# Kernel optimization log

Measured on AMD Instinct MI355X. Metric: run time of the kernel, lower is better.

The kernel has to match this reference:

```python
import jax, jax.numpy as jnp
import numpy as np

N = 2_000_000
H = 50
N_MID = 7  # number of Linear(50,50)+Tanh blocks


def setup_inputs() -> dict:
    key = jax.random.key(0)
    ks = jax.random.split(key, 9)
    s = 0.1  # small init scale to keep tanh out of saturation
    return {
        "x": jax.random.normal(ks[0], (N, 1), jnp.float32),
        "y": jax.random.normal(ks[1], (N, 1), jnp.float32),
        "z": jax.random.normal(ks[2], (N, 1), jnp.float32),
        "W_in": jax.random.normal(ks[3], (3, H), jnp.float32) * s,
        "b_in": jax.random.normal(ks[4], (H,), jnp.float32) * s,
        "W_mid": jax.random.normal(ks[5], (N_MID, H, H), jnp.float32) * s,
        "b_mid": jax.random.normal(ks[6], (N_MID, H), jnp.float32) * s,
        "W_out": jax.random.normal(ks[7], (H, 3), jnp.float32) * s,
        "b_out": jax.random.normal(ks[8], (3,), jnp.float32) * s,
    }


def reference(x, y, z, W_in, b_in, W_mid, b_mid, W_out, b_out):
    # Uin = hstack(x, y, z) -> [N, 3]
    Uin = jnp.concatenate([x, y, z], axis=1)
    h = jnp.tanh(Uin @ W_in + b_in)            # [N, 50]
    for i in range(N_MID):                      # fixed small layer count
        h = jnp.tanh(h @ W_mid[i] + b_mid[i])   # [N, 50]
    U = h @ W_out + b_out                       # [N, 3]
    return (U[:, 0:1], U[:, 1:2], U[:, 2:3])
```

## Files before the change

kernel.cpp:

```cpp
#include <hip/hip_runtime.h>

#define HID 50
#define NMID 7
#define NT 4
#define NS 2
#define PT 4

#define MID_ELEMS (NMID * NT * NS * 64 * 8)
#define IN_ELEMS  (NT * 64 * 8)
#define OUT_ELEMS (NS * 64 * 8)
#define W_HALFS   (MID_ELEMS + IN_ELEMS + OUT_ELEMS)

#define SCALE 2.8853900817779268f

typedef _Float16 half8  __attribute__((ext_vector_type(8)));
typedef float    f32x4  __attribute__((ext_vector_type(4)));

__device__ __forceinline__ unsigned short f16hi(float w) {
    _Float16 h = (_Float16)w;
    return __builtin_bit_cast(unsigned short, h);
}
__device__ __forceinline__ unsigned short f16lo(float w) {
    _Float16 h = (_Float16)w;
    _Float16 l = (_Float16)(w - (float)h);
    return __builtin_bit_cast(unsigned short, l);
}

__device__ __forceinline__ int kperm(int k) {
    int s = k >> 5, q = (k >> 3) & 3, j = k & 7;
    return 16 * (2 * s + (j >> 2)) + 4 * q + (j & 3);
}

__global__ void pack_params(const float* __restrict__ W_in, const float* __restrict__ b_in,
                            const float* __restrict__ W_mid, const float* __restrict__ b_mid,
                            const float* __restrict__ W_out, const float* __restrict__ b_out,
                            unsigned short* __restrict__ wp) {
    int e = blockIdx.x * 256 + threadIdx.x;
    if (e < MID_ELEMS) {
        int L = e / (NT * NS * 512), r1 = e % (NT * NS * 512);
        int t = r1 / (NS * 512),     r2 = r1 % (NS * 512);
        int s = r2 / 512,            r3 = r2 % 512;
        int l = r3 / 8,              j  = r3 % 8;
        int fo = t * 16 + (l & 15);
        int k  = s * 32 + ((l >> 4) << 3) + j;
        unsigned short bits = 0;
        if (fo < HID) {
            if (k == 62)      bits = f16hi(SCALE * b_mid[L * HID + fo]);
            else if (k == 63) bits = f16lo(SCALE * b_mid[L * HID + fo]);
            else {
                int fi = kperm(k);
                if (fi < HID) bits = f16hi(SCALE * W_mid[(L * HID + fi) * HID + fo]);
            }
        }
        wp[e] = bits;
    } else if (e < MID_ELEMS + IN_ELEMS) {
        int e2 = e - MID_ELEMS;
        int t = e2 / 512, r = e2 % 512, l = r / 8, j = r % 8;
        int fo = t * 16 + (l & 15);
        int q  = l >> 4;
        unsigned short bits = 0;
        if (fo < HID && q == 0) {
            if (j < 3)       bits = f16hi(SCALE * W_in[j * HID + fo]);
            else if (j < 6)  bits = f16hi(SCALE * W_in[(j - 3) * HID + fo]);
            else if (j == 6) bits = f16hi(SCALE * b_in[fo]);
            else             bits = f16lo(SCALE * b_in[fo]);
        }
        wp[e] = bits;
    } else if (e < W_HALFS) {
        int e3 = e - MID_ELEMS - IN_ELEMS;
        int s = e3 / 512, r = e3 % 512, l = r / 8, j = r % 8;
        int m = l & 15;
        int k = s * 32 + ((l >> 4) << 3) + j;
        unsigned short bits = 0;
        if (m < 3) {
            if (k == 62)      bits = f16hi(b_out[m]);
            else if (k == 63) bits = f16lo(b_out[m]);
            else {
                int fi = kperm(k);
                if (fi < HID) bits = f16hi(W_out[fi * 3 + m]);
            }
        }
        wp[e] = bits;
    }
}

__device__ __forceinline__ float tanh_e(float a) {
    float e = __builtin_amdgcn_exp2f(a);
    float r = __builtin_amdgcn_rcpf(e + 1.0f);
    return __builtin_fmaf(r, -2.0f, 1.0f);
}
__device__ __forceinline__ unsigned int pk2(float a, float b) {
    auto p = __builtin_amdgcn_cvt_pkrtz(a, b);
    return __builtin_bit_cast(unsigned int, p);
}
__device__ __forceinline__ half8 epi_full(const f32x4& c0, const f32x4& c1) {
    uint4 u;
    u.x = pk2(tanh_e(c0[0]), tanh_e(c0[1]));
    u.y = pk2(tanh_e(c0[2]), tanh_e(c0[3]));
    u.z = pk2(tanh_e(c1[0]), tanh_e(c1[1]));
    u.w = pk2(tanh_e(c1[2]), tanh_e(c1[3]));
    return __builtin_bit_cast(half8, u);
}
__device__ __forceinline__ half8 epi_tail(const f32x4& c2, const f32x4& c3) {
    uint4 u;
    u.x = pk2(tanh_e(c2[0]), tanh_e(c2[1]));
    u.y = pk2(tanh_e(c2[2]), tanh_e(c2[3]));
    u.z = pk2(tanh_e(c3[0]), tanh_e(c3[1]));
    u.w = 0x3C003C00u;
    return __builtin_bit_cast(half8, u);
}

__global__ __launch_bounds__(256, 4) void softmesh_mfma(
    const float* __restrict__ x, const float* __restrict__ y,
    const float* __restrict__ z,
    const unsigned short* __restrict__ wp,
    float* __restrict__ out, int n)
{
    const int tid  = threadIdx.x;
    const int wave = tid >> 6, lane = tid & 63;
    const int m = lane & 15, quad = lane >> 4;

    const int i0 = (blockIdx.x * 4 + wave) * 64;
    if (i0 >= n) return;

    const half8* __restrict__ Wm = (const half8*)wp;
    const half8* __restrict__ Wi = Wm + MID_ELEMS / 8;
    const half8* __restrict__ Wo = Wi + IN_ELEMS / 8;

    half8 Ain[NT];
#pragma unroll
    for (int t = 0; t < NT; ++t) Ain[t] = Wi[t * 64 + lane];
    half8 A[NT * NS];
#pragma unroll
    for (int i = 0; i < NT * NS; ++i) A[i] = Wm[i * 64 + lane];

    half8 B[PT][NS];

#pragma unroll
    for (int pt = 0; pt < PT; ++pt) {
        int idx = i0 + pt * 16 + m; if (idx >= n) idx = n - 1;
        half8 bf = {0, 0, 0, 0, 0, 0, 0, 0};
        if (quad == 0) {
            float xv = x[idx], yv = y[idx], zv = z[idx];
            _Float16 xh = (_Float16)xv, yh = (_Float16)yv, zh = (_Float16)zv;
            bf[0] = xh; bf[1] = yh; bf[2] = zh;
            bf[3] = (_Float16)(xv - (float)xh);
            bf[4] = (_Float16)(yv - (float)yh);
            bf[5] = (_Float16)(zv - (float)zh);
            bf[6] = (_Float16)1.0f; bf[7] = (_Float16)1.0f;
        }
        f32x4 cc[NT];
#pragma unroll
        for (int t = 0; t < NT; ++t) {
            f32x4 z4 = (f32x4){0.f, 0.f, 0.f, 0.f};
            cc[t] = __builtin_amdgcn_mfma_f32_16x16x32_f16(Ain[t], bf, z4, 0, 0, 0);
        }
        B[pt][0] = epi_full(cc[0], cc[1]);
        B[pt][1] = epi_tail(cc[2], cc[3]);
    }

#pragma unroll
    for (int L = 0; L < NMID; ++L) {
        half8 An[NT * NS];
        if (L < NMID - 1) {
#pragma unroll
            for (int i = 0; i < NT * NS; ++i) An[i] = Wm[((L + 1) * NT * NS + i) * 64 + lane];
        } else {
            An[0] = Wo[lane]; An[1] = Wo[64 + lane];
#pragma unroll
            for (int i = 2; i < NT * NS; ++i) An[i] = A[i];
        }
#pragma unroll
        for (int pt = 0; pt < PT; ++pt) {
            f32x4 cc[NT];
#pragma unroll
            for (int t = 0; t < NT; ++t) {
                f32x4 z4 = (f32x4){0.f, 0.f, 0.f, 0.f};
                f32x4 c = __builtin_amdgcn_mfma_f32_16x16x32_f16(A[t * NS + 0], B[pt][0], z4, 0, 0, 0);
                cc[t]   = __builtin_amdgcn_mfma_f32_16x16x32_f16(A[t * NS + 1], B[pt][1], c,  0, 0, 0);
            }
            B[pt][0] = epi_full(cc[0], cc[1]);
            B[pt][1] = epi_tail(cc[2], cc[3]);
        }
#pragma unroll
        for (int i = 0; i < NT * NS; ++i) A[i] = An[i];
    }

#pragma unroll
    for (int pt = 0; pt < PT; ++pt) {
        f32x4 z4 = (f32x4){0.f, 0.f, 0.f, 0.f};
        f32x4 c = __builtin_amdgcn_mfma_f32_16x16x32_f16(A[0], B[pt][0], z4, 0, 0, 0);
        c       = __builtin_amdgcn_mfma_f32_16x16x32_f16(A[1], B[pt][1], c,  0, 0, 0);
        if (quad == 0) {
            int idx = i0 + pt * 16 + m;
            if (idx < n) {
                out[idx] = c[0];
                out[(size_t)n + idx] = c[1];
                out[2 * (size_t)n + idx] = c[2];
            }
        }
    }
}

extern "C" void kernel_launch(void* const* d_in, const int* in_sizes, int n_in,
                              void* d_out, int out_size, void* d_ws, size_t ws_size,
                              hipStream_t stream) {
    const float* x     = (const float*)d_in[0];
    const float* y     = (const float*)d_in[1];
    const float* z     = (const float*)d_in[2];
    const float* W_in  = (const float*)d_in[3];
    const float* b_in  = (const float*)d_in[4];
    const float* W_mid = (const float*)d_in[5];
    const float* b_mid = (const float*)d_in[6];
    const float* W_out = (const float*)d_in[7];
    const float* b_out = (const float*)d_in[8];
    float* out = (float*)d_out;
    int n = in_sizes[0];

    unsigned short* wpp = (unsigned short*)d_ws;

    int pgrid = (W_HALFS + 255) / 256;
    pack_params<<<pgrid, 256, 0, stream>>>(W_in, b_in, W_mid, b_mid, W_out, b_out, wpp);

    int grid = (n + 255) / 256;
    softmesh_mfma<<<grid, 256, 0, stream>>>(x, y, z, wpp, out, n);
}
```

Baseline: 283.6 us.

## Fold tanh affine transform into weights and share reciprocal across value pairs

Represents each hidden activation as r = 1/(exp2(a)+0.5), with the 1-2r affine part folded into the packed weights and biases (negated weights, bias adjusted by column sums and -1). The per-element epilogue therefore drops its FMA. Two values share one reciprocal through a product trick, roughly halving the transcendental rcp count. It also remaps feature rows so only rows 0..48 and 52 are live. Risks include fp16 precision loss from larger folded biases, overflow of the product of two denominators, and extra column-sum work in the pack kernel.

```diff
diff --git a/kernel.cpp b/kernel.cpp
--- a/kernel.cpp
+++ b/kernel.cpp
@@ -15,6 +15,7 @@
 
 typedef _Float16 half8  __attribute__((ext_vector_type(8)));
 typedef float    f32x4  __attribute__((ext_vector_type(4)));
+typedef float    f32x2  __attribute__((ext_vector_type(2)));
 
 __device__ __forceinline__ unsigned short f16hi(float w) {
     _Float16 h = (_Float16)w;
@@ -29,6 +30,13 @@
 __device__ __forceinline__ int kperm(int k) {
     int s = k >> 5, q = (k >> 3) & 3, j = k & 7;
     return 16 * (2 * s + (j >> 2)) + 4 * q + (j & 3);
+}
+
+__device__ __forceinline__ int rowfeat(int rw) {
+    if (rw < 48) return rw;
+    if (rw == 48) return 48;
+    if (rw == 52) return 49;
+    return -1;
 }
 
 __global__ void pack_params(const float* __restrict__ W_in, const float* __restrict__ b_in,
@@ -41,29 +49,34 @@
         int t = r1 / (NS * 512),     r2 = r1 % (NS * 512);
         int s = r2 / 512,            r3 = r2 % 512;
         int l = r3 / 8,              j  = r3 % 8;
-        int fo = t * 16 + (l & 15);
+        int fo = rowfeat(t * 16 + (l & 15));
         int k  = s * 32 + ((l >> 4) << 3) + j;
         unsigned short bits = 0;
-        if (fo < HID) {
-            if (k == 62)      bits = f16hi(SCALE * b_mid[L * HID + fo]);
-            else if (k == 63) bits = f16lo(SCALE * b_mid[L * HID + fo]);
-            else {
-                int fi = kperm(k);
-                if (fi < HID) bits = f16hi(SCALE * W_mid[(L * HID + fi) * HID + fo]);
+        if (fo >= 0) {
+            if (k >= 62) {
+                float sum = b_mid[L * HID + fo];
+                for (int jj = 0; jj < HID; ++jj) sum += W_mid[(L * HID + jj) * HID + fo];
+                float v = SCALE * sum - 1.0f;
+                bits = (k == 62) ? f16hi(v) : f16lo(v);
+            } else {
+                int fi = rowfeat(kperm(k));
+                if (fi >= 0) bits = f16hi(-SCALE * W_mid[(L * HID + fi) * HID + fo]);
             }
         }
         wp[e] = bits;
     } else if (e < MID_ELEMS + IN_ELEMS) {
         int e2 = e - MID_ELEMS;
         int t = e2 / 512, r = e2 % 512, l = r / 8, j = r % 8;
-        int fo = t * 16 + (l & 15);
+        int fo = rowfeat(t * 16 + (l & 15));
         int q  = l >> 4;
         unsigned short bits = 0;
-        if (fo < HID && q == 0) {
+        if (fo >= 0 && q == 0) {
             if (j < 3)       bits = f16hi(SCALE * W_in[j * HID + fo]);
             else if (j < 6)  bits = f16hi(SCALE * W_in[(j - 3) * HID + fo]);
-            else if (j == 6) bits = f16hi(SCALE * b_in[fo]);
-            else             bits = f16lo(SCALE * b_in[fo]);
+            else {
+                float v = SCALE * b_in[fo] - 1.0f;
+                bits = (j == 6) ? f16hi(v) : f16lo(v);
+            }
         }
         wp[e] = bits;
     } else if (e < W_HALFS) {
@@ -73,39 +86,47 @@
         int k = s * 32 + ((l >> 4) << 3) + j;
         unsigned short bits = 0;
         if (m < 3) {
-            if (k == 62)      bits = f16hi(b_out[m]);
-            else if (k == 63) bits = f16lo(b_out[m]);
-            else {
-                int fi = kperm(k);
-                if (fi < HID) bits = f16hi(W_out[fi * 3 + m]);
+            if (k >= 62) {
+                float sum = b_out[m];
+                for (int jj = 0; jj < HID; ++jj) sum += W_out[jj * 3 + m];
+                bits = (k == 62) ? f16hi(sum) : f16lo(sum);
+            } else {
+                int fi = rowfeat(kperm(k));
+                if (fi >= 0) bits = f16hi(-W_out[fi * 3 + m]);
             }
         }
         wp[e] = bits;
     }
 }
 
-__device__ __forceinline__ float tanh_e(float a) {
-    float e = __builtin_amdgcn_exp2f(a);
-    float r = __builtin_amdgcn_rcpf(e + 1.0f);
-    return __builtin_fmaf(r, -2.0f, 1.0f);
-}
 __device__ __forceinline__ unsigned int pk2(float a, float b) {
     auto p = __builtin_amdgcn_cvt_pkrtz(a, b);
     return __builtin_bit_cast(unsigned int, p);
 }
+__device__ __forceinline__ unsigned int rr_pair(float a0, float a1) {
+    f32x2 e;
+    e[0] = __builtin_amdgcn_exp2f(a0);
+    e[1] = __builtin_amdgcn_exp2f(a1);
+    f32x2 d = e + 0.5f;
+    float inv = __builtin_amdgcn_rcpf(d[0] * d[1]);
+    f32x2 r = inv * __builtin_shufflevector(d, d, 1, 0);
+    return pk2(r[0], r[1]);
+}
 __device__ __forceinline__ half8 epi_full(const f32x4& c0, const f32x4& c1) {
     uint4 u;
-    u.x = pk2(tanh_e(c0[0]), tanh_e(c0[1]));
-    u.y = pk2(tanh_e(c0[2]), tanh_e(c0[3]));
-    u.z = pk2(tanh_e(c1[0]), tanh_e(c1[1]));
-    u.w = pk2(tanh_e(c1[2]), tanh_e(c1[3]));
+    u.x = rr_pair(c0[0], c0[1]);
+    u.y = rr_pair(c0[2], c0[3]);
+    u.z = rr_pair(c1[0], c1[1]);
+    u.w = rr_pair(c1[2], c1[3]);
     return __builtin_bit_cast(half8, u);
 }
 __device__ __forceinline__ half8 epi_tail(const f32x4& c2, const f32x4& c3) {
     uint4 u;
-    u.x = pk2(tanh_e(c2[0]), tanh_e(c2[1]));
-    u.y = pk2(tanh_e(c2[2]), tanh_e(c2[3]));
-    u.z = pk2(tanh_e(c3[0]), tanh_e(c3[1]));
+    u.x = rr_pair(c2[0], c2[1]);
+    u.y = rr_pair(c2[2], c2[3]);
+    float e = __builtin_amdgcn_exp2f(c3[0]);
+    float r = __builtin_amdgcn_rcpf(e + 0.5f);
+    u.z = pk2(r, 1.0f);
     u.w = 0x3C003C00u;
     return __builtin_bit_cast(half8, u);
 }
@@ -138,7 +159,7 @@
 
 #pragma unroll
     for (int pt = 0; pt < PT; ++pt) {
-        int idx = i0 + pt * 16 + m; if (idx >= n) idx = n - 1;
+        int idx = min(i0 + pt * 16 + m, n - 1);
         half8 bf = {0, 0, 0, 0, 0, 0, 0, 0};
         if (quad == 0) {
             float xv = x[idx], yv = y[idx], zv = z[idx];
```

After: 264.6 us. 6.7% less time.
